# Kernel optimization log

Measured on AMD Instinct MI355X. Metric: run time of the kernel, lower is better.

## Reference

```python
import jax, jax.numpy as jnp
import numpy as np

N, E, F, H, C = 50000, 800000, 64, 64, 10


def setup_inputs() -> dict:
    key = jax.random.key(0)
    ks = jax.random.split(key, 9)
    x = jax.random.normal(ks[0], (N, F), dtype=jnp.float32)
    edge_index = jax.random.randint(ks[1], (2, E), 0, N, dtype=jnp.int64)
    s_f = 1.0 / np.sqrt(F)
    s_h = 1.0 / np.sqrt(H)
    return {
        "x": x,
        "edge_index": edge_index,
        # ChebConv(F->H, K=1): only Theta_0
        "W1_0": jax.random.normal(ks[2], (F, H), dtype=jnp.float32) * s_f,
        "b1": jnp.zeros((H,), dtype=jnp.float32),
        # ChebConv(H->H, K=2): Theta_0, Theta_1
        "W2_0": jax.random.normal(ks[3], (H, H), dtype=jnp.float32) * s_h,
        "W2_1": jax.random.normal(ks[4], (H, H), dtype=jnp.float32) * s_h,
        "b2": jnp.zeros((H,), dtype=jnp.float32),
        # final Linear(H->C)
        "Wl": jax.random.normal(ks[5], (H, C), dtype=jnp.float32) * s_h,
        "bl": jnp.zeros((C,), dtype=jnp.float32),
    }


def reference(x, edge_index, W1_0, b1, W2_0, W2_1, b2, Wl, bl):
    n = x.shape[0]
    src, dst = edge_index[0], edge_index[1]
    # Scaled Laplacian (PyG ChebConv, sym norm, lambda_max=2.0):
    # L_hat = -D^{-1/2} A D^{-1/2}  (self-loop terms cancel: +1 scaled, then -1 added)
    deg = jax.ops.segment_sum(jnp.ones((src.shape[0],), dtype=x.dtype), src,
                              num_segments=n)
    dis = jnp.where(deg > 0, jax.lax.rsqrt(jnp.maximum(deg, 1.0)), 0.0)
    w = -(dis[src] * dis[dst])  # [E]

    def lap(h):  # L_hat @ h via edge-wise gather/scatter
        return jax.ops.segment_sum(w[:, None] * h[src], dst, num_segments=n)

    # conv1 (K=1): T0 = x only -> plain linear
    h = jax.nn.relu(x @ W1_0 + b1)
    # dropout is identity in eval mode
    x_res = h
    # conv2 (K=2): T0 = h, T1 = L_hat h
    h2 = jax.nn.relu(h @ W2_0 + lap(h) @ W2_1 + b2)
    out = (h2 + x_res) @ Wl + bl
    return jax.nn.log_softmax(out, axis=1)
```

## Files before the change

### kernel.cpp

```cpp
#include <hip/hip_runtime.h>
#include <math.h>
#include <stdint.h>


#define NBKT 256
#define BCAP 5120
#define CHUNK 2048

__device__ __forceinline__ unsigned short f2bf(float f) {
    uint32_t u; __builtin_memcpy(&u, &f, 4);
    u += 0x7fffu + ((u >> 16) & 1u);
    return (unsigned short)(u >> 16);
}
__device__ __forceinline__ float bf2f(unsigned short s) {
    uint32_t u = (uint32_t)s << 16; float f; __builtin_memcpy(&f, &u, 4);
    return f;
}
__device__ __forceinline__ int xcc_id() {
    int x;
    asm("s_getreg_b32 %0, hwreg(HW_REG_XCC_ID)" : "=s"(x));
    return x;
}

__global__ __launch_bounds__(256) void binA_kernel(const int* __restrict__ ei,
                                                   int* __restrict__ gcur,
                                                   uint32_t* __restrict__ pairs,
                                                   int* __restrict__ degI8,
                                                   int E, int n) {
    __shared__ uint32_t stage[CHUNK];
    __shared__ int cnt[NBKT], obase[NBKT], goff[NBKT], curs[NBKT];
    __shared__ int wpart[4], stot;
    int t = threadIdx.x, lane = t & 63, wv = t >> 6;
    int e0 = blockIdx.x * CHUNK;
    int* degP = degI8 + (size_t)(xcc_id() & 7) * n;
    int s[8], d[8];
    bool val[8];
#pragma unroll
    for (int j = 0; j < 8; ++j) {
        int e = e0 + j * 256 + t;
        val[j] = e < E;
        s[j] = val[j] ? ei[e] : 0;
        d[j] = val[j] ? ei[E + e] : 0;
    }
    cnt[t] = 0;
    __syncthreads();
#pragma unroll
    for (int j = 0; j < 8; ++j)
        if (val[j]) {
            atomicAdd(&cnt[d[j] >> 8], 1);
            atomicAdd(&degP[s[j]], 1);
        }
    __syncthreads();
    int cv = cnt[t];
    int v = cv;
#pragma unroll
    for (int dd = 1; dd < 64; dd <<= 1) {
        int u = __shfl_up(v, dd);
        if (lane >= dd) v += u;
    }
    if (lane == 63) wpart[wv] = v;
    __syncthreads();
    if (t == 0) {
        int r = 0;
#pragma unroll
        for (int w = 0; w < 4; ++w) { int tmp = wpart[w]; wpart[w] = r; r += tmp; }
        stot = r;
    }
    __syncthreads();
    int eb = wpart[wv] + v - cv;
    obase[t] = eb;
    curs[t] = eb;
    goff[t] = (cv > 0) ? atomicAdd(&gcur[t], cv) : 0;
    __syncthreads();
#pragma unroll
    for (int j = 0; j < 8; ++j)
        if (val[j]) {
            int b = d[j] >> 8;
            int pos = atomicAdd(&curs[b], 1);
            stage[pos] = ((uint32_t)d[j] << 16) | (uint32_t)s[j];
        }
    __syncthreads();
    int tot = stot;
    for (int k = t; k < tot; k += 256) {
        uint32_t u = stage[k];
        int b = (int)(u >> 24);
        int slot = goff[b] + (k - obase[b]);
        if (slot < BCAP) pairs[(size_t)b * BCAP + slot] = u;
    }
}

__global__ __launch_bounds__(256) void binB_kernel(const int* __restrict__ gcur,
                                                   const uint32_t* __restrict__ pairs,
                                                   int* __restrict__ csr,
                                                   int* __restrict__ rowptr,
                                                   int* __restrict__ cntD,
                                                   const int* __restrict__ degI8,
                                                   float* __restrict__ dis, int n) {
    __shared__ int hist[NBKT], obase[NBKT], curs[NBKT];
    __shared__ int wpart[4];
    int t = threadIdx.x, lane = t & 63, wv = t >> 6;
    int b = blockIdx.x;
    {
        int node = b * 256 + t;
        if (node < n) {
            int dsum = 0;
#pragma unroll
            for (int j = 0; j < 8; ++j) dsum += degI8[(size_t)j * n + node];
            dis[node] = (dsum > 0) ? rsqrtf((float)dsum) : 0.0f;
        }
    }
    int nb = gcur[b]; if (nb > BCAP) nb = BCAP;
    hist[t] = 0;
    __syncthreads();
    const uint32_t* bp = pairs + (size_t)b * BCAP;
    for (int k = t; k < nb; k += 256) {
        int ld = (int)((bp[k] >> 16) & 255);
        atomicAdd(&hist[ld], 1);
    }
    __syncthreads();
    int cv = hist[t];
    int v = cv;
#pragma unroll
    for (int dd = 1; dd < 64; dd <<= 1) {
        int u = __shfl_up(v, dd);
        if (lane >= dd) v += u;
    }
    if (lane == 63) wpart[wv] = v;
    __syncthreads();
    if (t == 0) {
        int r = 0;
#pragma unroll
        for (int w = 0; w < 4; ++w) { int tmp = wpart[w]; wpart[w] = r; r += tmp; }
    }
    __syncthreads();
    int eb = wpart[wv] + v - cv;
    obase[t] = eb;
    curs[t] = eb;
    int node = b * 256 + t;
    if (node < n) {
        rowptr[node] = b * BCAP + eb;
        cntD[node] = cv;
    }
    __syncthreads();
    for (int k = t; k < nb; k += 256) {
        uint32_t u = bp[k];
        int ld = (int)((u >> 16) & 255);
        int pos = atomicAdd(&curs[ld], 1);
        csr[(size_t)b * BCAP + pos] = (int)(u & 0xffffu);
    }
}

__global__ __launch_bounds__(256) void gemm3_kernel(const float* __restrict__ x,
                                                    const float* __restrict__ W1,
                                                    const float* __restrict__ b1,
                                                    const float* __restrict__ W20,
                                                    const float* __restrict__ W21,
                                                    const float* __restrict__ b2,
                                                    const float* __restrict__ dis,
                                                    unsigned short* __restrict__ h16,
                                                    unsigned short* __restrict__ p16,
                                                    unsigned short* __restrict__ g16,
                                                    int n) {
    __shared__ __align__(16) float sA[64][68];
    __shared__ __align__(16) float sW1[64][64];
    __shared__ __align__(16) float sW20[64][64];
    __shared__ __align__(16) float sW21[64][64];
    int t = threadIdx.x;
    for (int i = t; i < 4096; i += 256) {
        sW1[i >> 6][i & 63] = W1[i];
        sW20[i >> 6][i & 63] = W20[i];
        sW21[i >> 6][i & 63] = W21[i];
    }
    int r0 = blockIdx.x * 64;
    {
        int rr0 = t >> 4, k0 = (t & 15) * 4;
        for (int rr = rr0; rr < 64; rr += 16) {
            int grow = r0 + rr;
            float4 v = make_float4(0.f, 0.f, 0.f, 0.f);
            if (grow < n) v = *(const float4*)&x[(size_t)grow * 64 + k0];
            sA[k0][rr] = v.x; sA[k0 + 1][rr] = v.y;
            sA[k0 + 2][rr] = v.z; sA[k0 + 3][rr] = v.w;
        }
    }
    __syncthreads();
    int tr = t >> 4, tc = t & 15;

    float acc[4][4] = {};
    for (int k = 0; k < 64; ++k) {
        float4 a = *(const float4*)&sA[k][tr * 4];
        float4 b = *(const float4*)&sW1[k][tc * 4];
        float av[4] = {a.x, a.y, a.z, a.w};
        float bv[4] = {b.x, b.y, b.z, b.w};
#pragma unroll
        for (int i = 0; i < 4; ++i)
#pragma unroll
            for (int j = 0; j < 4; ++j) acc[i][j] = fmaf(av[i], bv[j], acc[i][j]);
    }
    float4 bv1 = *(const float4*)&b1[tc * 4];
    float hv[4][4];
#pragma unroll
    for (int i = 0; i < 4; ++i) {
        hv[i][0] = fmaxf(acc[i][0] + bv1.x, 0.f);
        hv[i][1] = fmaxf(acc[i][1] + bv1.y, 0.f);
        hv[i][2] = fmaxf(acc[i][2] + bv1.z, 0.f);
        hv[i][3] = fmaxf(acc[i][3] + bv1.w, 0.f);
    }
#pragma unroll
    for (int i = 0; i < 4; ++i) {
        int grow = r0 + tr * 4 + i;
        if (grow < n) {
            ushort4 o;
            o.x = f2bf(hv[i][0]); o.y = f2bf(hv[i][1]);
            o.z = f2bf(hv[i][2]); o.w = f2bf(hv[i][3]);
            *(ushort4*)&h16[(size_t)grow * 64 + tc * 4] = o;
        }
    }
    __syncthreads();
#pragma unroll
    for (int i = 0; i < 4; ++i)
#pragma unroll
        for (int j = 0; j < 4; ++j) sA[tc * 4 + j][tr * 4 + i] = hv[i][j];
    __syncthreads();

    float accP[4][4] = {}, accG[4][4] = {};
    for (int k = 0; k < 64; ++k) {
        float4 a = *(const float4*)&sA[k][tr * 4];
        float4 bp = *(const float4*)&sW20[k][tc * 4];
        float4 bg = *(const float4*)&sW21[k][tc * 4];
        float av[4] = {a.x, a.y, a.z, a.w};
        float bpv[4] = {bp.x, bp.y, bp.z, bp.w};
        float bgv[4] = {bg.x, bg.y, bg.z, bg.w};
#pragma unroll
        for (int i = 0; i < 4; ++i)
#pragma unroll
            for (int j = 0; j < 4; ++j) {
                accP[i][j] = fmaf(av[i], bpv[j], accP[i][j]);
                accG[i][j] = fmaf(av[i], bgv[j], accG[i][j]);
            }
    }
    float4 bv2 = *(const float4*)&b2[tc * 4];
#pragma unroll
    for (int i = 0; i < 4; ++i) {
        int grow = r0 + tr * 4 + i;
        if (grow < n) {
            float dr = dis[grow];
            ushort4 op, og;
            op.x = f2bf(accP[i][0] + bv2.x); op.y = f2bf(accP[i][1] + bv2.y);
            op.z = f2bf(accP[i][2] + bv2.z); op.w = f2bf(accP[i][3] + bv2.w);
            og.x = f2bf(dr * accG[i][0]); og.y = f2bf(dr * accG[i][1]);
            og.z = f2bf(dr * accG[i][2]); og.w = f2bf(dr * accG[i][3]);
            *(ushort4*)&p16[(size_t)grow * 64 + tc * 4] = op;
            *(ushort4*)&g16[(size_t)grow * 64 + tc * 4] = og;
        }
    }
}

__global__ __launch_bounds__(256, 8) void gather_out_kernel(
        const int* __restrict__ rowptr, const int* __restrict__ cntD,
        const int* __restrict__ csr, const float* __restrict__ dis,
        const unsigned short* __restrict__ g16, const unsigned short* __restrict__ p16,
        const unsigned short* __restrict__ h16, const float* __restrict__ Wl,
        const float* __restrict__ bl, float* __restrict__ out, int n) {
    int c = threadIdx.x & 63;
    int wid = __builtin_amdgcn_readfirstlane(threadIdx.x >> 6);
    int row = blockIdx.x * 4 + wid;
    if (row >= n) return;
    int m = cntD[row], rs = rowptr[row];
    float disd = dis[row];
    float pv = bf2f(p16[(size_t)row * 64 + c]);
    float hv = bf2f(h16[(size_t)row * 64 + c]);

    float a0 = 0.f, a1 = 0.f, a2 = 0.f, a3 = 0.f;
    float a4 = 0.f, a5 = 0.f, a6 = 0.f, a7 = 0.f;
    int k = 0;
    for (; k + 16 <= m; k += 16) {
        int s0 = csr[rs + k],      s1 = csr[rs + k + 1];
        int s2 = csr[rs + k + 2],  s3 = csr[rs + k + 3];
        int s4 = csr[rs + k + 4],  s5 = csr[rs + k + 5];
        int s6 = csr[rs + k + 6],  s7 = csr[rs + k + 7];
        int s8 = csr[rs + k + 8],  s9 = csr[rs + k + 9];
        int sa = csr[rs + k + 10], sb = csr[rs + k + 11];
        int sc = csr[rs + k + 12], sd = csr[rs + k + 13];
        int se = csr[rs + k + 14], sf = csr[rs + k + 15];
        float v0 = bf2f(g16[(size_t)s0 * 64 + c]);
        float v1 = bf2f(g16[(size_t)s1 * 64 + c]);
        float v2 = bf2f(g16[(size_t)s2 * 64 + c]);
        float v3 = bf2f(g16[(size_t)s3 * 64 + c]);
        float v4 = bf2f(g16[(size_t)s4 * 64 + c]);
        float v5 = bf2f(g16[(size_t)s5 * 64 + c]);
        float v6 = bf2f(g16[(size_t)s6 * 64 + c]);
        float v7 = bf2f(g16[(size_t)s7 * 64 + c]);
        float v8 = bf2f(g16[(size_t)s8 * 64 + c]);
        float v9 = bf2f(g16[(size_t)s9 * 64 + c]);
        float va = bf2f(g16[(size_t)sa * 64 + c]);
        float vb = bf2f(g16[(size_t)sb * 64 + c]);
        float vc = bf2f(g16[(size_t)sc * 64 + c]);
        float vd = bf2f(g16[(size_t)sd * 64 + c]);
        float ve = bf2f(g16[(size_t)se * 64 + c]);
        float vf = bf2f(g16[(size_t)sf * 64 + c]);
        a0 += v0 + v8; a1 += v1 + v9; a2 += v2 + va; a3 += v3 + vb;
        a4 += v4 + vc; a5 += v5 + vd; a6 += v6 + ve; a7 += v7 + vf;
    }
    for (; k + 4 <= m; k += 4) {
        int s0 = csr[rs + k],     s1 = csr[rs + k + 1];
        int s2 = csr[rs + k + 2], s3 = csr[rs + k + 3];
        a0 += bf2f(g16[(size_t)s0 * 64 + c]);
        a1 += bf2f(g16[(size_t)s1 * 64 + c]);
        a2 += bf2f(g16[(size_t)s2 * 64 + c]);
        a3 += bf2f(g16[(size_t)s3 * 64 + c]);
    }
    for (; k < m; ++k) {
        int s0 = csr[rs + k];
        a0 += bf2f(g16[(size_t)s0 * 64 + c]);
    }
    float lv = -disd * (((a0 + a1) + (a2 + a3)) + ((a4 + a5) + (a6 + a7)));
    float h2 = fmaxf(pv + lv, 0.f) + hv;

    float wl[10];
#pragma unroll
    for (int j = 0; j < 10; ++j) wl[j] = Wl[c * 10 + j];
    float mmax = -1e30f, myout = 0.f;
#pragma unroll
    for (int j = 0; j < 10; ++j) {
        float p = h2 * wl[j];
#pragma unroll
        for (int mk = 1; mk < 64; mk <<= 1) p += __shfl_xor(p, mk);
        p += bl[j];
        if (c == j) myout = p;
        mmax = fmaxf(mmax, p);
    }
    float ev = (c < 10) ? expf(myout - mmax) : 0.f;
#pragma unroll
    for (int mk = 1; mk < 64; mk <<= 1) ev += __shfl_xor(ev, mk);
    if (c < 10) out[(size_t)row * 10 + c] = myout - mmax - logf(ev);
}

extern "C" void kernel_launch(void* const* d_in, const int* in_sizes, int n_in,
                              void* d_out, int out_size, void* d_ws, size_t ws_size,
                              hipStream_t stream) {
    const float* x   = (const float*)d_in[0];
    const int*   ei  = (const int*)d_in[1];
    const float* W1  = (const float*)d_in[2];
    const float* b1  = (const float*)d_in[3];
    const float* W20 = (const float*)d_in[4];
    const float* W21 = (const float*)d_in[5];
    const float* b2  = (const float*)d_in[6];
    const float* Wl  = (const float*)d_in[7];
    const float* bl  = (const float*)d_in[8];
    float* out = (float*)d_out;

    int n = in_sizes[0] / 64;
    int E = in_sizes[1] / 2;

    char* ws = (char*)d_ws;
    size_t off = 0;
    auto alloc = [&](size_t bytes) {
        void* p = ws + off;
        off = (off + bytes + 255) & ~(size_t)255;
        return p;
    };
    int*       gcur   = (int*)alloc((size_t)NBKT * 4);
    uint32_t*  pairs  = (uint32_t*)alloc((size_t)NBKT * BCAP * 4);
    int*       csr    = (int*)alloc((size_t)NBKT * BCAP * 4);
    int*       rowptr = (int*)alloc((size_t)n * 4);
    int*       cntD   = (int*)alloc((size_t)n * 4);
    int*       degI8  = (int*)alloc((size_t)n * 8 * 4);
    float*     dis    = (float*)alloc((size_t)n * 4);
    unsigned short* h16 = (unsigned short*)alloc((size_t)n * 64 * 2);
    unsigned short* p16 = (unsigned short*)alloc((size_t)n * 64 * 2);
    unsigned short* g16 = (unsigned short*)alloc((size_t)n * 64 * 2);

    hipMemsetAsync(gcur, 0, (size_t)NBKT * 4, stream);
    hipMemsetAsync(degI8, 0, (size_t)n * 8 * 4, stream);

    int nchunk = (E + CHUNK - 1) / CHUNK;
    binA_kernel<<<nchunk, 256, 0, stream>>>(ei, gcur, pairs, degI8, E, n);
    binB_kernel<<<NBKT, 256, 0, stream>>>(gcur, pairs, csr, rowptr, cntD, degI8, dis, n);
    gemm3_kernel<<<(n + 63) / 64, 256, 0, stream>>>(x, W1, b1, W20, W21, b2, dis,
                                                    h16, p16, g16, n);
    gather_out_kernel<<<(n + 3) / 4, 256, 0, stream>>>(rowptr, cntD, csr, dis, g16,
                                                       p16, h16, Wl, bl, out, n);
}
```

Baseline: 197.5 us.

## Partition CSR neighbors by source half and batch final linear through shared memory

binB now places neighbors with source index below n/2 at the front of each row segment and the rest at the back, and records a per-node low count. The gather kernel walks the two segments separately, so gathers from the two halves of g16 are grouped, which may improve cache locality, for example across XCC-local L2 slices. The final 64x10 linear layer and log-softmax are moved from per-wave shuffle reductions to a shared-memory dot product using a transposed Wl, with one thread per output. This adds block barriers and splits the unrolled loop into two segments, giving more tail iterations per row.

```diff
diff --git a/kernel.cpp b/kernel.cpp
--- a/kernel.cpp
+++ b/kernel.cpp
@@ -94,9 +94,11 @@
                                                    int* __restrict__ csr,
                                                    int* __restrict__ rowptr,
                                                    int* __restrict__ cntD,
+                                                   int* __restrict__ cntLow,
                                                    const int* __restrict__ degI8,
-                                                   float* __restrict__ dis, int n) {
-    __shared__ int hist[NBKT], obase[NBKT], curs[NBKT];
+                                                   float* __restrict__ dis,
+                                                   int n, int half) {
+    __shared__ int hist[NBKT], obase[NBKT], cursL[NBKT], cursH[NBKT];
     __shared__ int wpart[4];
     int t = threadIdx.x, lane = t & 63, wv = t >> 6;
     int b = blockIdx.x;
@@ -135,7 +137,8 @@
     __syncthreads();
     int eb = wpart[wv] + v - cv;
     obase[t] = eb;
-    curs[t] = eb;
+    cursL[t] = eb;
+    cursH[t] = eb + cv;
     int node = b * 256 + t;
     if (node < n) {
         rowptr[node] = b * BCAP + eb;
@@ -145,9 +148,14 @@
     for (int k = t; k < nb; k += 256) {
         uint32_t u = bp[k];
         int ld = (int)((u >> 16) & 255);
-        int pos = atomicAdd(&curs[ld], 1);
-        csr[(size_t)b * BCAP + pos] = (int)(u & 0xffffu);
-    }
+        int src = (int)(u & 0xffffu);
+        int pos;
+        if (src < half) pos = atomicAdd(&cursL[ld], 1);
+        else            pos = atomicSub(&cursH[ld], 1) - 1;
+        csr[(size_t)b * BCAP + pos] = src;
+    }
+    __syncthreads();
+    if (node < n) cntLow[node] = cursL[t] - obase[t];
 }
 
 __global__ __launch_bounds__(256) void gemm3_kernel(const float* __restrict__ x,
@@ -255,84 +263,115 @@
     }
 }
 
+#define GATHER_SEG(K0, K1)                                                  \
+    {                                                                        \
+        int k = (K0);                                                        \
+        for (; k + 16 <= (K1); k += 16) {                                    \
+            int s0 = csr[rs + k],      s1 = csr[rs + k + 1];                 \
+            int s2 = csr[rs + k + 2],  s3 = csr[rs + k + 3];                 \
+            int s4 = csr[rs + k + 4],  s5 = csr[rs + k + 5];                 \
+            int s6 = csr[rs + k + 6],  s7 = csr[rs + k + 7];                 \
+            int s8 = csr[rs + k + 8],  s9 = csr[rs + k + 9];                 \
+            int sa = csr[rs + k + 10], sb = csr[rs + k + 11];                \
+            int sc = csr[rs + k + 12], sd = csr[rs + k + 13];                \
+            int se = csr[rs + k + 14], sf = csr[rs + k + 15];                \
+            float v0 = bf2f(g16[(size_t)s0 * 64 + c]);                       \
+            float v1 = bf2f(g16[(size_t)s1 * 64 + c]);                       \
+            float v2 = bf2f(g16[(size_t)s2 * 64 + c]);                       \
+            float v3 = bf2f(g16[(size_t)s3 * 64 + c]);                       \
+            float v4 = bf2f(g16[(size_t)s4 * 64 + c]);                       \
+            float v5 = bf2f(g16[(size_t)s5 * 64 + c]);                       \
+            float v6 = bf2f(g16[(size_t)s6 * 64 + c]);                       \
+            float v7 = bf2f(g16[(size_t)s7 * 64 + c]);                       \
+            float v8 = bf2f(g16[(size_t)s8 * 64 + c]);                       \
+            float v9 = bf2f(g16[(size_t)s9 * 64 + c]);                       \
+            float va = bf2f(g16[(size_t)sa * 64 + c]);                       \
+            float vb = bf2f(g16[(size_t)sb * 64 + c]);                       \
+            float vc = bf2f(g16[(size_t)sc * 64 + c]);                       \
+            float vd = bf2f(g16[(size_t)sd * 64 + c]);                       \
+            float ve = bf2f(g16[(size_t)se * 64 + c]);                       \
+            float vf = bf2f(g16[(size_t)sf * 64 + c]);                       \
+            a0 += v0 + v8; a1 += v1 + v9; a2 += v2 + va; a3 += v3 + vb;      \
+            a4 += v4 + vc; a5 += v5 + vd; a6 += v6 + ve; a7 += v7 + vf;      \
+        }                                                                    \
+        for (; k + 4 <= (K1); k += 4) {                                      \
+            int s0 = csr[rs + k],     s1 = csr[rs + k + 1];                  \
+            int s2 = csr[rs + k + 2], s3 = csr[rs + k + 3];                  \
+            a0 += bf2f(g16[(size_t)s0 * 64 + c]);                            \
+            a1 += bf2f(g16[(size_t)s1 * 64 + c]);                            \
+            a2 += bf2f(g16[(size_t)s2 * 64 + c]);                            \
+            a3 += bf2f(g16[(size_t)s3 * 64 + c]);                            \
+        }                                                                    \
+        for (; k < (K1); ++k) {                                              \
+            int s0 = csr[rs + k];                                            \
+            a0 += bf2f(g16[(size_t)s0 * 64 + c]);                            \
+        }                                                                    \
+    }
+
 __global__ __launch_bounds__(256, 8) void gather_out_kernel(
         const int* __restrict__ rowptr, const int* __restrict__ cntD,
-        const int* __restrict__ csr, const float* __restrict__ dis,
+        const int* __restrict__ cntLow, const int* __restrict__ csr,
+        const float* __restrict__ dis,
         const unsigned short* __restrict__ g16, const unsigned short* __restrict__ p16,
         const unsigned short* __restrict__ h16, const float* __restrict__ Wl,
         const float* __restrict__ bl, float* __restrict__ out, int n) {
-    int c = threadIdx.x & 63;
-    int wid = __builtin_amdgcn_readfirstlane(threadIdx.x >> 6);
+    __shared__ __align__(16) float so[4][68];
+    __shared__ __align__(16) float sWlT[10][68];
+    __shared__ float sout[4][12];
+    int t = threadIdx.x;
+    if (t < 160) {
+        float4 w = *(const float4*)&Wl[t * 4];
+        int i0 = t * 4;
+        sWlT[i0 % 10][i0 / 10] = w.x;
+        sWlT[(i0 + 1) % 10][(i0 + 1) / 10] = w.y;
+        sWlT[(i0 + 2) % 10][(i0 + 2) / 10] = w.z;
+        sWlT[(i0 + 3) % 10][(i0 + 3) / 10] = w.w;
+    }
+    int c = t & 63;
+    int wid = __builtin_amdgcn_readfirstlane(t >> 6);
     int row = blockIdx.x * 4 + wid;
-    if (row >= n) return;
-    int m = cntD[row], rs = rowptr[row];
-    float disd = dis[row];
-    float pv = bf2f(p16[(size_t)row * 64 + c]);
-    float hv = bf2f(h16[(size_t)row * 64 + c]);
-
-    float a0 = 0.f, a1 = 0.f, a2 = 0.f, a3 = 0.f;
-    float a4 = 0.f, a5 = 0.f, a6 = 0.f, a7 = 0.f;
-    int k = 0;
-    for (; k + 16 <= m; k += 16) {
-        int s0 = csr[rs + k],      s1 = csr[rs + k + 1];
-        int s2 = csr[rs + k + 2],  s3 = csr[rs + k + 3];
-        int s4 = csr[rs + k + 4],  s5 = csr[rs + k + 5];
-        int s6 = csr[rs + k + 6],  s7 = csr[rs + k + 7];
-        int s8 = csr[rs + k + 8],  s9 = csr[rs + k + 9];
-        int sa = csr[rs + k + 10], sb = csr[rs + k + 11];
-        int sc = csr[rs + k + 12], sd = csr[rs + k + 13];
-        int se = csr[rs + k + 14], sf = csr[rs + k + 15];
-        float v0 = bf2f(g16[(size_t)s0 * 64 + c]);
-        float v1 = bf2f(g16[(size_t)s1 * 64 + c]);
-        float v2 = bf2f(g16[(size_t)s2 * 64 + c]);
-        float v3 = bf2f(g16[(size_t)s3 * 64 + c]);
-        float v4 = bf2f(g16[(size_t)s4 * 64 + c]);
-        float v5 = bf2f(g16[(size_t)s5 * 64 + c]);
-        float v6 = bf2f(g16[(size_t)s6 * 64 + c]);
-        float v7 = bf2f(g16[(size_t)s7 * 64 + c]);
-        float v8 = bf2f(g16[(size_t)s8 * 64 + c]);
-        float v9 = bf2f(g16[(size_t)s9 * 64 + c]);
-        float va = bf2f(g16[(size_t)sa * 64 + c]);
-        float vb = bf2f(g16[(size_t)sb * 64 + c]);
-        float vc = bf2f(g16[(size_t)sc * 64 + c]);
-        float vd = bf2f(g16[(size_t)sd * 64 + c]);
-        float ve = bf2f(g16[(size_t)se * 64 + c]);
-        float vf = bf2f(g16[(size_t)sf * 64 + c]);
-        a0 += v0 + v8; a1 += v1 + v9; a2 += v2 + va; a3 += v3 + vb;
-        a4 += v4 + vc; a5 += v5 + vd; a6 += v6 + ve; a7 += v7 + vf;
-    }
-    for (; k + 4 <= m; k += 4) {
-        int s0 = csr[rs + k],     s1 = csr[rs + k + 1];
-        int s2 = csr[rs + k + 2], s3 = csr[rs + k + 3];
-        a0 += bf2f(g16[(size_t)s0 * 64 + c]);
-        a1 += bf2f(g16[(size_t)s1 * 64 + c]);
-        a2 += bf2f(g16[(size_t)s2 * 64 + c]);
-        a3 += bf2f(g16[(size_t)s3 * 64 + c]);
-    }
-    for (; k < m; ++k) {
-        int s0 = csr[rs + k];
-        a0 += bf2f(g16[(size_t)s0 * 64 + c]);
-    }
-    float lv = -disd * (((a0 + a1) + (a2 + a3)) + ((a4 + a5) + (a6 + a7)));
-    float h2 = fmaxf(pv + lv, 0.f) + hv;
-
-    float wl[10];
-#pragma unroll
-    for (int j = 0; j < 10; ++j) wl[j] = Wl[c * 10 + j];
-    float mmax = -1e30f, myout = 0.f;
-#pragma unroll
-    for (int j = 0; j < 10; ++j) {
-        float p = h2 * wl[j];
-#pragma unroll
-        for (int mk = 1; mk < 64; mk <<= 1) p += __shfl_xor(p, mk);
-        p += bl[j];
-        if (c == j) myout = p;
-        mmax = fmaxf(mmax, p);
-    }
-    float ev = (c < 10) ? expf(myout - mmax) : 0.f;
-#pragma unroll
-    for (int mk = 1; mk < 64; mk <<= 1) ev += __shfl_xor(ev, mk);
-    if (c < 10) out[(size_t)row * 10 + c] = myout - mmax - logf(ev);
+    if (row < n) {
+        int m = cntD[row], rs = rowptr[row], mL = cntLow[row];
+        float disd = dis[row];
+        float a0 = 0.f, a1 = 0.f, a2 = 0.f, a3 = 0.f;
+        float a4 = 0.f, a5 = 0.f, a6 = 0.f, a7 = 0.f;
+        GATHER_SEG(0, mL);
+        GATHER_SEG(mL, m);
+        float lv = -disd * (((a0 + a1) + (a2 + a3)) + ((a4 + a5) + (a6 + a7)));
+        float pv = bf2f(p16[(size_t)row * 64 + c]);
+        float hv = bf2f(h16[(size_t)row * 64 + c]);
+        so[wid][c] = fmaxf(pv + lv, 0.f) + hv;
+    }
+    __syncthreads();
+    if (t < 40) {
+        int r = t / 10, j = t % 10;
+        float acc = bl[j];
+#pragma unroll
+        for (int k0 = 0; k0 < 64; k0 += 4) {
+            float4 a = *(const float4*)&so[r][k0];
+            float4 b = *(const float4*)&sWlT[j][k0];
+            acc = fmaf(a.x, b.x, acc);
+            acc = fmaf(a.y, b.y, acc);
+            acc = fmaf(a.z, b.z, acc);
+            acc = fmaf(a.w, b.w, acc);
+        }
+        sout[r][j] = acc;
+    }
+    __syncthreads();
+    if (t < 64) {
+        int r = t >> 4, l16 = t & 15;
+        float v = (l16 < 10) ? sout[r][l16] : -1e30f;
+        float mm = v;
+#pragma unroll
+        for (int d = 1; d < 16; d <<= 1) mm = fmaxf(mm, __shfl_xor(mm, d, 16));
+        float e = (l16 < 10) ? expf(v - mm) : 0.f;
+        float ss = e;
+#pragma unroll
+        for (int d = 1; d < 16; d <<= 1) ss += __shfl_xor(ss, d, 16);
+        int grow = blockIdx.x * 4 + r;
+        if (grow < n && l16 < 10)
+            out[(size_t)grow * 10 + l16] = v - mm - logf(ss);
+    }
 }
 
 extern "C" void kernel_launch(void* const* d_in, const int* in_sizes, int n_in,
@@ -364,6 +403,7 @@
     int*       csr    = (int*)alloc((size_t)NBKT * BCAP * 4);
     int*       rowptr = (int*)alloc((size_t)n * 4);
     int*       cntD   = (int*)alloc((size_t)n * 4);
+    int*       cntLow = (int*)alloc((size_t)n * 4);
     int*       degI8  = (int*)alloc((size_t)n * 8 * 4);
     float*     dis    = (float*)alloc((size_t)n * 4);
     unsigned short* h16 = (unsigned short*)alloc((size_t)n * 64 * 2);
@@ -375,9 +415,11 @@
 
     int nchunk = (E + CHUNK - 1) / CHUNK;
     binA_kernel<<<nchunk, 256, 0, stream>>>(ei, gcur, pairs, degI8, E, n);
-    binB_kernel<<<NBKT, 256, 0, stream>>>(gcur, pairs, csr, rowptr, cntD, degI8, dis, n);
+    binB_kernel<<<NBKT, 256, 0, stream>>>(gcur, pairs, csr, rowptr, cntD, cntLow,
+                                          degI8, dis, n, n / 2);
     gemm3_kernel<<<(n + 63) / 64, 256, 0, stream>>>(x, W1, b1, W20, W21, b2, dis,
                                                     h16, p16, g16, n);
-    gather_out_kernel<<<(n + 3) / 4, 256, 0, stream>>>(rowptr, cntD, csr, dis, g16,
-                                                       p16, h16, Wl, bl, out, n);
-}
+    gather_out_kernel<<<(n + 3) / 4, 256, 0, stream>>>(rowptr, cntD, cntLow, csr,
+                                                       dis, g16, p16, h16, Wl, bl,
+                                                       out, n);
+}
```

New measurement: 198.5 us. About the same (+0.5%).
